# Performance work log

Measured on AMD Instinct MI355X. Metric: run time of the kernel, lower is better.

Reference implementation:

```python
import jax, jax.numpy as jnp
from jax import lax
import numpy as np

BETA = 0.25
K = 64   # num_embeddings
D = 64   # embedding_dim (must equal K per module's view(-1, D))
HID = 128
RES = 64
N_RES = 2


def _conv(x, w, b=None, stride=1, pad=0):
    y = lax.conv_general_dilated(x, w, (stride, stride), [(pad, pad), (pad, pad)],
                                 dimension_numbers=('NCHW', 'OIHW', 'NCHW'))
    if b is not None:
        y = y + b[None, :, None, None]
    return y


def _deconv(x, w, b, stride, pad):
    # torch ConvTranspose2d weight is (Cin, Cout, k, k); emulate via lhs-dilated conv with flipped kernel
    k = w.shape[2]
    p = k - 1 - pad
    w2 = jnp.transpose(w[:, :, ::-1, ::-1], (1, 0, 2, 3))  # -> (Cout, Cin, k, k)
    y = lax.conv_general_dilated(x, w2, (1, 1), [(p, p), (p, p)], lhs_dilation=(stride, stride),
                                 dimension_numbers=('NCHW', 'OIHW', 'NCHW'))
    return y + b[None, :, None, None]


def _res_block(x, w1, w2):
    # [Residual_Layer]*N_RES shares ONE set of weights; in-place ReLU means skip adds relu(x)
    for _ in range(N_RES):
        r = jax.nn.relu(x)
        h = _conv(r, w1, pad=1)
        h = jax.nn.relu(h)
        h = _conv(h, w2)
        x = r + h
    return jax.nn.relu(x)


def setup_inputs() -> dict:
    key = jax.random.key(0)
    ks = jax.random.split(key, 16)
    f32 = jnp.float32
    s = 0.05
    inp = {
        'x': jax.random.normal(ks[0], (32, 1, 256, 256), f32),
        # encoder
        'enc_c1_w': jax.random.normal(ks[1], (HID // 2, 1, 4, 4), f32) * s,
        'enc_c1_b': jnp.zeros((HID // 2,), f32),
        'enc_c2_w': jax.random.normal(ks[2], (HID, HID // 2, 4, 4), f32) * s,
        'enc_c2_b': jnp.zeros((HID,), f32),
        'enc_c3_w': jax.random.normal(ks[3], (HID, HID, 3, 3), f32) * s,
        'enc_c3_b': jnp.zeros((HID,), f32),
        'enc_r1_w': jax.random.normal(ks[4], (RES, HID, 3, 3), f32) * s,
        'enc_r2_w': jax.random.normal(ks[5], (HID, RES, 1, 1), f32) * s,
        # pre-VQ 1x1 conv: hidden -> K channels
        'vqc_w': jax.random.normal(ks[6], (K, HID, 1, 1), f32) * s,
        'vqc_b': jnp.zeros((K,), f32),
        # codebook, uniform(-1/K, 1/K)
        'emb': jax.random.uniform(ks[7], (K, D), f32, -1.0 / K, 1.0 / K),
        # decoder (ConvTranspose2d weights are (Cin, Cout, k, k))
        'dec_c1_w': jax.random.normal(ks[8], (D, HID, 3, 3), f32) * s,
        'dec_c1_b': jnp.zeros((HID,), f32),
        'dec_r1_w': jax.random.normal(ks[9], (RES, HID, 3, 3), f32) * s,
        'dec_r2_w': jax.random.normal(ks[10], (HID, RES, 1, 1), f32) * s,
        'dec_c2_w': jax.random.normal(ks[11], (HID, HID // 2, 4, 4), f32) * s,
        'dec_c2_b': jnp.zeros((HID // 2,), f32),
        'dec_c3_w': jax.random.normal(ks[12], (HID // 2, 1, 4, 4), f32) * s,
        'dec_c3_b': jnp.zeros((1,), f32),
    }
    return inp


def reference(x, enc_c1_w, enc_c1_b, enc_c2_w, enc_c2_b, enc_c3_w, enc_c3_b,
              enc_r1_w, enc_r2_w, vqc_w, vqc_b, emb,
              dec_c1_w, dec_c1_b, dec_r1_w, dec_r2_w, dec_c2_w, dec_c2_b, dec_c3_w, dec_c3_b):
    # ---- encoder ----
    h = jax.nn.relu(_conv(x, enc_c1_w, enc_c1_b, stride=2, pad=1))
    h = jax.nn.relu(_conv(h, enc_c2_w, enc_c2_b, stride=2, pad=1))
    h = _conv(h, enc_c3_w, enc_c3_b, pad=1)
    h = _res_block(h, enc_r1_w, enc_r2_w)
    z = _conv(h, vqc_w, vqc_b)  # (B, K, 64, 64)

    # ---- VQ ----
    zt = jnp.transpose(z, (0, 2, 3, 1))            # (B, H, W, D)
    flat = zt.reshape(-1, D)                        # (N, D)
    dist = (jnp.sum(flat ** 2, axis=1, keepdims=True)
            + jnp.sum(emb ** 2, axis=1)
            - 2.0 * flat @ emb.T)                   # (N, K)
    idx = jnp.argmin(dist, axis=1)                  # (N,)
    onehot = jax.nn.one_hot(idx, K, dtype=flat.dtype)
    q = (onehot @ emb).reshape(zt.shape)
    commitment = jnp.mean((lax.stop_gradient(q) - zt) ** 2)
    embedding_l = jnp.mean((q - lax.stop_gradient(zt)) ** 2)
    loss = commitment * BETA + embedding_l
    q_st = zt + lax.stop_gradient(q - zt)           # straight-through
    mean_enc = jnp.mean(onehot, axis=0)
    perplexity = jnp.exp(-jnp.sum(mean_enc * jnp.log(mean_enc + 1e-10)))
    qn = jnp.transpose(q_st, (0, 3, 1, 2))          # (B, D, 64, 64)

    # ---- decoder ----
    d = _deconv(qn, dec_c1_w, dec_c1_b, 1, 1)
    d = _res_block(d, dec_r1_w, dec_r2_w)
    d = jax.nn.relu(_deconv(d, dec_c2_w, dec_c2_b, 2, 1))
    x_re = jnp.tanh(_deconv(d, dec_c3_w, dec_c3_b, 2, 1))
    return (loss, x_re, perplexity, qn)
```

## Files before the change

### kernel.cpp

```cpp
#include <hip/hip_runtime.h>
#include <cmath>


static constexpr int NPOS  = 131072;
static constexpr long long NELEM = 8388608;

typedef __attribute__((ext_vector_type(8))) short short8;
typedef __attribute__((ext_vector_type(8))) unsigned short ushort8;
typedef __attribute__((ext_vector_type(4))) float f32x4;

__device__ __forceinline__ unsigned short f2bf(float f) {
  unsigned int x = __float_as_uint(f);
  unsigned int r = (x + 0x7fffu + ((x >> 16) & 1u)) >> 16;
  return (unsigned short)r;
}
__device__ __forceinline__ float bf2f(unsigned short u) {
  return __uint_as_float(((unsigned int)u) << 16);
}
__device__ __forceinline__ void split2(float v, unsigned short& h, unsigned short& l) {
  unsigned short hh = f2bf(v);
  h = hh;
  l = f2bf(v - bf2f(hh));
}

__global__ void __launch_bounds__(256) enc1_t(
    const float* __restrict__ in, const float* __restrict__ w,
    const float* __restrict__ bias,
    unsigned short* __restrict__ outh, unsigned short* __restrict__ outl)
{
  int tid = threadIdx.x;
  int rr = tid >> 7, ox = tid & 127;
  int oy  = blockIdx.x * 2 + rr;
  int oc0 = blockIdx.y * 16;
  int b   = blockIdx.z;

  const float* pl = in + (size_t)b * 65536;
  float v[16];
  #pragma unroll
  for (int ky = 0; ky < 4; ++ky) {
    int iy = 2 * oy - 1 + ky;
    #pragma unroll
    for (int kx = 0; kx < 4; ++kx) {
      int ix = 2 * ox - 1 + kx;
      v[ky * 4 + kx] = (iy >= 0 && iy < 256 && ix >= 0 && ix < 256)
                       ? pl[iy * 256 + ix] : 0.f;
    }
  }
  float acc[16];
  #pragma unroll
  for (int o = 0; o < 16; ++o) acc[o] = bias[oc0 + o];
  #pragma unroll
  for (int t = 0; t < 16; ++t)
    #pragma unroll
    for (int o = 0; o < 16; ++o)
      acc[o] += v[t] * w[(size_t)(oc0 + o) * 16 + t];

  size_t o = ((size_t)b * 16900 + (size_t)(oy + 1) * 130 + (ox + 1)) * 64 + oc0;
  ushort8 h0, h1, l0, l1;
  #pragma unroll
  for (int k = 0; k < 8; ++k) {
    unsigned short hh, ll;
    split2(fmaxf(acc[k], 0.f), hh, ll);      h0[k] = hh; l0[k] = ll;
    split2(fmaxf(acc[k + 8], 0.f), hh, ll);  h1[k] = hh; l1[k] = ll;
  }
  *(ushort8*)(outh + o)     = h0;
  *(ushort8*)(outh + o + 8) = h1;
  *(ushort8*)(outl + o)     = l0;
  *(ushort8*)(outl + o + 8) = l1;
}

template<int IC, int OC, int MODE, bool BIAS, bool RELU>
__global__ void __launch_bounds__(256) mfma_enc(
    const unsigned short* __restrict__ inh, const unsigned short* __restrict__ inl,
    const unsigned short* __restrict__ wh, const unsigned short* __restrict__ wl,
    const float* __restrict__ bias,
    const unsigned short* __restrict__ skh, const unsigned short* __restrict__ skl,
    unsigned short* __restrict__ outh, unsigned short* __restrict__ outl)
{
  constexpr int OM = OC / 16;
  constexpr int NT = (MODE == 0) ? 9 : ((MODE == 1) ? 16 : 1);
  constexpr int IW = (MODE == 1) ? 130 : 66;
  const int in_ss  = IW * IW * IC;
  const int out_ss = 4356 * OC;
  const int tid = threadIdx.x;
  const int wv = tid >> 6, lane = tid & 63;
  const int quad = lane >> 4, l15 = lane & 15;
  const int b = blockIdx.z;
  const int y = blockIdx.x * 4 + wv;
  int xs[4];
  #pragma unroll
  for (int j = 0; j < 4; ++j) xs[j] = j * 16 + l15;
  const unsigned short* ibh = inh + (size_t)b * in_ss;
  const unsigned short* ibl = inl + (size_t)b * in_ss;

  f32x4 acc[OM][4];
  #pragma unroll
  for (int m = 0; m < OM; ++m) {
    const int oc0 = m * 16 + quad * 4;
    f32x4 ini = {0.f, 0.f, 0.f, 0.f};
    if (BIAS) {
      float4 bs = *(const float4*)(bias + oc0);
      ini[0] = bs.x; ini[1] = bs.y; ini[2] = bs.z; ini[3] = bs.w;
    }
    #pragma unroll
    for (int j = 0; j < 4; ++j) {
      f32x4 a = ini;
      if (MODE == 2) {
        size_t s = (size_t)b * out_ss + ((size_t)(y + 1) * 66 + (xs[j] + 1)) * OC + oc0;
        ushort4 sh = *(const ushort4*)(skh + s);
        ushort4 sl = *(const ushort4*)(skl + s);
        a[0] += bf2f(sh.x) + bf2f(sl.x);
        a[1] += bf2f(sh.y) + bf2f(sl.y);
        a[2] += bf2f(sh.z) + bf2f(sl.z);
        a[3] += bf2f(sh.w) + bf2f(sl.w);
      }
      acc[m][j] = a;
    }
  }

  for (int t = 0; t < NT; ++t) {
    int off[4];
    #pragma unroll
    for (int j = 0; j < 4; ++j) {
      if (MODE == 1)
        off[j] = ((2 * y + (t >> 2)) * 130 + (2 * xs[j] + (t & 3))) * IC;
      else if (MODE == 0) {
        int dy = t / 3 - 1, dx = t % 3 - 1;
        off[j] = ((y + dy + 1) * 66 + (xs[j] + dx + 1)) * IC;
      } else
        off[j] = ((y + 1) * 66 + (xs[j] + 1)) * IC;
    }
    const unsigned short* wrh = wh + (size_t)t * OC * IC + l15 * IC + quad * 8;
    const unsigned short* wrl = wl + (size_t)t * OC * IC + l15 * IC + quad * 8;
    #pragma unroll
    for (int k0 = 0; k0 < IC; k0 += 32) {
      short8 bh[4], bl[4];
      #pragma unroll
      for (int j = 0; j < 4; ++j) {
        bh[j] = *(const short8*)(ibh + off[j] + quad * 8 + k0);
        bl[j] = *(const short8*)(ibl + off[j] + quad * 8 + k0);
      }
      #pragma unroll
      for (int m = 0; m < OM; ++m) {
        short8 ah = *(const short8*)(wrh + (size_t)m * 16 * IC + k0);
        short8 al = *(const short8*)(wrl + (size_t)m * 16 * IC + k0);
        #pragma unroll
        for (int j = 0; j < 4; ++j) {
          acc[m][j] = __builtin_amdgcn_mfma_f32_16x16x32_bf16(ah, bh[j], acc[m][j], 0, 0, 0);
          acc[m][j] = __builtin_amdgcn_mfma_f32_16x16x32_bf16(ah, bl[j], acc[m][j], 0, 0, 0);
          acc[m][j] = __builtin_amdgcn_mfma_f32_16x16x32_bf16(al, bh[j], acc[m][j], 0, 0, 0);
        }
      }
    }
  }

  #pragma unroll
  for (int m = 0; m < OM; ++m) {
    const int oc0 = m * 16 + quad * 4;
    #pragma unroll
    for (int j = 0; j < 4; ++j) {
      size_t o = (size_t)b * out_ss + ((size_t)(y + 1) * 66 + (xs[j] + 1)) * OC + oc0;
      ushort4 h4, l4;
      unsigned short hh, ll;
      float v;
      v = acc[m][j][0]; if (RELU) v = fmaxf(v, 0.f); split2(v, hh, ll); h4.x = hh; l4.x = ll;
      v = acc[m][j][1]; if (RELU) v = fmaxf(v, 0.f); split2(v, hh, ll); h4.y = hh; l4.y = ll;
      v = acc[m][j][2]; if (RELU) v = fmaxf(v, 0.f); split2(v, hh, ll); h4.z = hh; l4.z = ll;
      v = acc[m][j][3]; if (RELU) v = fmaxf(v, 0.f); split2(v, hh, ll); h4.w = hh; l4.w = ll;
      *(ushort4*)(outh + o) = h4;
      *(ushort4*)(outl + o) = l4;
    }
  }
}

__global__ void __launch_bounds__(256) vq_mfma(
    const unsigned short* __restrict__ xh, const unsigned short* __restrict__ xl,
    const unsigned short* __restrict__ wvh, const unsigned short* __restrict__ wvl,
    const unsigned short* __restrict__ evh, const unsigned short* __restrict__ evl,
    const float* __restrict__ emb, const float* __restrict__ e2,
    const float* __restrict__ vb,
    float* __restrict__ qn, unsigned short* __restrict__ dqb,
    float* __restrict__ sum_sq, int* __restrict__ hist)
{
  __shared__ float zsh[4][16][65];
  __shared__ int lh[64];
  const int tid = threadIdx.x;
  const int wv = tid >> 6, lane = tid & 63;
  const int quad = lane >> 4, l15 = lane & 15;
  const int y = blockIdx.x;
  const int b = blockIdx.z;
  const int x = wv * 16 + l15;
  if (tid < 64) lh[tid] = 0;

  f32x4 zacc[4];
  #pragma unroll
  for (int m = 0; m < 4; ++m) {
    float4 bv = *(const float4*)(vb + m * 16 + quad * 4);
    zacc[m][0] = bv.x; zacc[m][1] = bv.y; zacc[m][2] = bv.z; zacc[m][3] = bv.w;
  }
  size_t xoff = ((size_t)b * 4356 + (size_t)(y + 1) * 66 + (x + 1)) * 128;
  #pragma unroll
  for (int k0 = 0; k0 < 128; k0 += 32) {
    short8 bh = *(const short8*)(xh + xoff + k0 + quad * 8);
    short8 bl = *(const short8*)(xl + xoff + k0 + quad * 8);
    #pragma unroll
    for (int m = 0; m < 4; ++m) {
      short8 ah = *(const short8*)(wvh + (size_t)(m * 16 + l15) * 128 + k0 + quad * 8);
      short8 al = *(const short8*)(wvl + (size_t)(m * 16 + l15) * 128 + k0 + quad * 8);
      zacc[m] = __builtin_amdgcn_mfma_f32_16x16x32_bf16(ah, bh, zacc[m], 0, 0, 0);
      zacc[m] = __builtin_amdgcn_mfma_f32_16x16x32_bf16(ah, bl, zacc[m], 0, 0, 0);
      zacc[m] = __builtin_amdgcn_mfma_f32_16x16x32_bf16(al, bh, zacc[m], 0, 0, 0);
    }
  }

  float z2p = 0.f;
  #pragma unroll
  for (int m = 0; m < 4; ++m)
    #pragma unroll
    for (int r = 0; r < 4; ++r) {
      float zv = zacc[m][r];
      zsh[wv][l15][m * 16 + quad * 4 + r] = zv;
      z2p += zv * zv;
    }
  z2p += __shfl_xor(z2p, 16);
  z2p += __shfl_xor(z2p, 32);
  __syncthreads();

  f32x4 dacc[4];
  #pragma unroll
  for (int m = 0; m < 4; ++m) { dacc[m][0]=0.f; dacc[m][1]=0.f; dacc[m][2]=0.f; dacc[m][3]=0.f; }
  #pragma unroll
  for (int k0 = 0; k0 < 64; k0 += 32) {
    short8 bh, bl;
    #pragma unroll
    for (int j = 0; j < 8; ++j) {
      float zv = zsh[wv][l15][k0 + quad * 8 + j];
      unsigned short hh, ll;
      split2(zv, hh, ll);
      bh[j] = (short)hh; bl[j] = (short)ll;
    }
    #pragma unroll
    for (int m = 0; m < 4; ++m) {
      short8 ah = *(const short8*)(evh + (size_t)(m * 16 + l15) * 64 + k0 + quad * 8);
      short8 al = *(const short8*)(evl + (size_t)(m * 16 + l15) * 64 + k0 + quad * 8);
      dacc[m] = __builtin_amdgcn_mfma_f32_16x16x32_bf16(ah, bh, dacc[m], 0, 0, 0);
      dacc[m] = __builtin_amdgcn_mfma_f32_16x16x32_bf16(ah, bl, dacc[m], 0, 0, 0);
      dacc[m] = __builtin_amdgcn_mfma_f32_16x16x32_bf16(al, bh, dacc[m], 0, 0, 0);
    }
  }

  float best = INFINITY;
  int bidx = 64;
  #pragma unroll
  for (int m = 0; m < 4; ++m) {
    float4 e2v = *(const float4*)(e2 + m * 16 + quad * 4);
    #pragma unroll
    for (int r = 0; r < 4; ++r) {
      float e2s = (r == 0) ? e2v.x : (r == 1) ? e2v.y : (r == 2) ? e2v.z : e2v.w;
      float d = z2p + e2s - 2.f * dacc[m][r];
      int code = m * 16 + quad * 4 + r;
      if (d < best || (d == best && code < bidx)) { best = d; bidx = code; }
    }
  }
  {
    float ob = __shfl_xor(best, 16);
    int   oi = __shfl_xor(bidx, 16);
    if (ob < best || (ob == best && oi < bidx)) { best = ob; bidx = oi; }
    ob = __shfl_xor(best, 32);
    oi = __shfl_xor(bidx, 32);
    if (ob < best || (ob == best && oi < bidx)) { best = ob; bidx = oi; }
  }

  float ev[16];
  #pragma unroll
  for (int i = 0; i < 4; ++i) {
    float4 t = *(const float4*)(emb + (size_t)bidx * 64 + quad * 16 + i * 4);
    ev[i * 4] = t.x; ev[i * 4 + 1] = t.y; ev[i * 4 + 2] = t.z; ev[i * 4 + 3] = t.w;
  }
  float sq = 0.f;
  #pragma unroll
  for (int i = 0; i < 16; ++i) {
    float zv = zsh[wv][l15][quad * 16 + i];
    float df = ev[i] - zv;
    sq += df * df;
  }
  #pragma unroll
  for (int off = 1; off < 64; off <<= 1) sq += __shfl_xor(sq, off);
  if (lane == 0) atomicAdd(sum_sq, sq);
  if (quad == 0) atomicAdd(&lh[bidx], 1);

  int pos = y * 64 + x;
  float* qb = qn + (size_t)b * 262144 + (size_t)(quad * 16) * 4096 + pos;
  #pragma unroll
  for (int i = 0; i < 16; ++i) qb[(size_t)i * 4096] = ev[i];

  unsigned short* dq = dqb + ((size_t)b * 4356 + (size_t)(y + 1) * 66 + (x + 1)) * 64 + quad * 16;
  ushort8 d0, d1;
  #pragma unroll
  for (int i = 0; i < 8; ++i) { d0[i] = f2bf(ev[i]); d1[i] = f2bf(ev[i + 8]); }
  *(ushort8*)dq = d0;
  *(ushort8*)(dq + 8) = d1;

  __syncthreads();
  if (tid < 64) atomicAdd(&hist[tid], lh[tid]);
}

template<int IC, int OC, int MODE, bool HAS_BIAS, bool HAS_SKIP, bool RELU>
__global__ void __launch_bounds__(256) mfma_conv(
    const unsigned short* __restrict__ in, const unsigned short* __restrict__ wt,
    const float* __restrict__ bias, const unsigned short* __restrict__ skip,
    unsigned short* __restrict__ out, int in_ss, int out_ss)
{
  constexpr int OM = OC / 16;
  constexpr int NT = (MODE == 0) ? 9 : ((MODE == 1) ? 4 : 1);
  int ry = 0, rx = 0;
  if (MODE == 1) {
    int p = blockIdx.y;
    ry = p >> 1; rx = p & 1;
    wt  += (size_t)p * 4 * OC * IC;
    out += (size_t)p * 4356 * OC;
  }
  const int tid = threadIdx.x;
  const int wv = tid >> 6, lane = tid & 63;
  const int quad = lane >> 4, l15 = lane & 15;
  const int b = blockIdx.z;
  const int y = blockIdx.x * 4 + wv;
  int xs[4];
  #pragma unroll
  for (int j = 0; j < 4; ++j) xs[j] = j * 16 + l15;
  const unsigned short* inb = in + (size_t)b * (size_t)in_ss;

  f32x4 acc[OM][4];
  #pragma unroll
  for (int m = 0; m < OM; ++m) {
    const int oc0 = m * 16 + quad * 4;
    f32x4 ini = {0.f, 0.f, 0.f, 0.f};
    if (HAS_BIAS) {
      float4 bs = *(const float4*)(bias + oc0);
      ini[0] = bs.x; ini[1] = bs.y; ini[2] = bs.z; ini[3] = bs.w;
    }
    #pragma unroll
    for (int j = 0; j < 4; ++j) {
      f32x4 a = ini;
      if (HAS_SKIP) {
        size_t s = (size_t)b * (size_t)out_ss + ((size_t)(y + 1) * 66 + (xs[j] + 1)) * OC + oc0;
        ushort4 sv = *(const ushort4*)(skip + s);
        a[0] += bf2f(sv.x); a[1] += bf2f(sv.y); a[2] += bf2f(sv.z); a[3] += bf2f(sv.w);
      }
      acc[m][j] = a;
    }
  }

  #pragma unroll
  for (int t = 0; t < NT; ++t) {
    const int dy = (MODE == 0) ? (t / 3 - 1) : ((MODE == 1) ? (ry - (t >> 1)) : 0);
    const int dx = (MODE == 0) ? (t % 3 - 1) : ((MODE == 1) ? (rx - (t & 1)) : 0);
    const unsigned short* wr = wt + (size_t)t * OC * IC + (size_t)l15 * IC + quad * 8;
    #pragma unroll
    for (int k0 = 0; k0 < IC; k0 += 32) {
      short8 fb[4];
      #pragma unroll
      for (int j = 0; j < 4; ++j)
        fb[j] = *(const short8*)(inb + ((size_t)(y + dy + 1) * 66 + (xs[j] + dx + 1)) * IC + quad * 8 + k0);
      #pragma unroll
      for (int m = 0; m < OM; ++m) {
        short8 fa = *(const short8*)(wr + (size_t)m * 16 * IC + k0);
        #pragma unroll
        for (int j = 0; j < 4; ++j)
          acc[m][j] = __builtin_amdgcn_mfma_f32_16x16x32_bf16(fa, fb[j], acc[m][j], 0, 0, 0);
      }
    }
  }

  #pragma unroll
  for (int m = 0; m < OM; ++m) {
    const int oc0 = m * 16 + quad * 4;
    #pragma unroll
    for (int j = 0; j < 4; ++j) {
      unsigned short* o = out + (size_t)b * (size_t)out_ss
                        + ((size_t)(y + 1) * 66 + (xs[j] + 1)) * OC + oc0;
      ushort4 u4;
      float v;
      v = acc[m][j][0]; if (RELU) v = fmaxf(v, 0.f); u4.x = f2bf(v);
      v = acc[m][j][1]; if (RELU) v = fmaxf(v, 0.f); u4.y = f2bf(v);
      v = acc[m][j][2]; if (RELU) v = fmaxf(v, 0.f); u4.z = f2bf(v);
      v = acc[m][j][3]; if (RELU) v = fmaxf(v, 0.f); u4.w = f2bf(v);
      *(ushort4*)o = u4;
    }
  }
}

__global__ void __launch_bounds__(256) dec3_t(
    const unsigned short* __restrict__ p4, const float* __restrict__ w,
    const float* __restrict__ bias, float* __restrict__ out)
{
  int tid = threadIdx.x;
  int yr = tid >> 7, x = tid & 127;
  int y  = blockIdx.x * 2 + yr;
  int b  = blockIdx.z;

  const int kt[2][2] = {{1, 3}, {0, 2}};
  const int dt[2][2] = {{1, 0}, {2, 1}};

  const unsigned short* base[9];
  #pragma unroll
  for (int dy = 0; dy < 3; ++dy) {
    int iy = y + dy - 1;
    int py = iy & 1, u = iy >> 1;
    #pragma unroll
    for (int dx = 0; dx < 3; ++dx) {
      int ix = x + dx - 1;
      int px = ix & 1, v = ix >> 1;
      base[dy * 3 + dx] = p4 + ((size_t)(b * 4 + py * 2 + px) * 4356
                                + (size_t)(u + 1) * 66 + (v + 1)) * 64;
    }
  }

  float acc[4] = {0.f, 0.f, 0.f, 0.f};
  for (int oct = 0; oct < 8; ++oct) {
    ushort8 s[9];
    #pragma unroll
    for (int t = 0; t < 9; ++t)
      s[t] = *(const ushort8*)(base[t] + oct * 8);

    #pragma unroll
    for (int j = 0; j < 8; ++j) {
      const float* wp = w + (size_t)(oct * 8 + j) * 16;
      float v9[9];
      #pragma unroll
      for (int t = 0; t < 9; ++t) v9[t] = bf2f(s[t][j]);
      #pragma unroll
      for (int ry = 0; ry < 2; ++ry)
        #pragma unroll
        for (int rx = 0; rx < 2; ++rx)
          #pragma unroll
          for (int a = 0; a < 2; ++a)
            #pragma unroll
            for (int c2 = 0; c2 < 2; ++c2)
              acc[ry * 2 + rx] += v9[dt[ry][a] * 3 + dt[rx][c2]]
                                * wp[kt[ry][a] * 4 + kt[rx][c2]];
    }
  }

  float b0 = bias[0];
  float* ob = out + (size_t)b * 65536;
  #pragma unroll
  for (int ry = 0; ry < 2; ++ry)
    #pragma unroll
    for (int rx = 0; rx < 2; ++rx)
      ob[(2 * y + ry) * 256 + 2 * x + rx] = tanhf(acc[ry * 2 + rx] + b0);
}

struct RingArgs {
  unsigned short* p[5];
  int icl[5];
  int H[5];
  int planes[5];
};
__global__ void rings_k(RingArgs a)
{
  int bi = blockIdx.y;
  if ((int)blockIdx.x >= a.planes[bi]) return;
  int H = a.H[bi];
  int icl = a.icl[bi];
  int C = 1 << icl;
  unsigned short* pl = a.p[bi] + (size_t)blockIdx.x * H * H * C;
  int cells = 4 * H - 4;
  int total = cells * C;
  for (int idx = threadIdx.x; idx < total; idx += 256) {
    int cell = idx >> icl;
    int e = idx & (C - 1);
    int row, col;
    if (cell < H)             { row = 0;     col = cell; }
    else if (cell < 2 * H)    { row = H - 1; col = cell - H; }
    else if (cell < 2 * H + (H - 2)) { row = cell - 2 * H + 1; col = 0; }
    else                      { row = cell - 2 * H - (H - 2) + 1; col = H - 1; }
    pl[((size_t)row * H + col) * C + e] = 0;
  }
}

__global__ void repack_k(const float* __restrict__ c1w, const float* __restrict__ r1w,
                         const float* __restrict__ r2w, const float* __restrict__ c2w,
                         unsigned short* __restrict__ W)
{
  int idx = blockIdx.x * 256 + threadIdx.x;
  if (idx >= 286720) return;
  float val;
  if (idx < 73728) {
    int t = idx / 8192, rem = idx & 8191;
    int oc = rem >> 6, ic = rem & 63;
    int ky = t / 3, kx = t - ky * 3;
    val = c1w[((ic * 128 + oc) * 3 + (2 - ky)) * 3 + (2 - kx)];
  } else if (idx < 147456) {
    int j = idx - 73728;
    int t = j / 8192, rem = j & 8191;
    int oc = rem >> 7, ic = rem & 127;
    int ky = t / 3, kx = t - ky * 3;
    val = r1w[((oc * 128 + ic) * 3 + ky) * 3 + kx];
  } else if (idx < 155648) {
    int j = idx - 147456;
    int oc = j >> 6, ic = j & 63;
    val = r2w[oc * 64 + ic];
  } else {
    int j = idx - 155648;
    int p = j >> 15;
    int t2 = (j >> 13) & 3;
    int oc = (j >> 7) & 63;
    int ic = j & 127;
    int ry = p >> 1, rx = p & 1;
    int aY = t2 >> 1, aX = t2 & 1;
    int ky = aY ? (3 - ry) : (1 - ry);
    int kx = aX ? (3 - rx) : (1 - rx);
    val = c2w[((ic * 64 + oc) * 4 + ky) * 4 + kx];
  }
  W[idx] = f2bf(val);
}

__global__ void repack_enc_k(const float* __restrict__ c2w, const float* __restrict__ c3w,
                             const float* __restrict__ r1w, const float* __restrict__ r2w,
                             unsigned short* __restrict__ Wh, unsigned short* __restrict__ Wl)
{
  int idx = blockIdx.x * 256 + threadIdx.x;
  if (idx >= 360448) return;
  float val;
  if (idx < 131072) {
    int t = idx >> 13;
    int rem = idx & 8191;
    int oc = rem >> 6, ic = rem & 63;
    val = c2w[(((size_t)oc * 64 + ic) << 4) + t];
  } else if (idx < 278528) {
    int j = idx - 131072;
    int t = j / 16384;
    int rem = j & 16383;
    int oc = rem >> 7, ic = rem & 127;
    val = c3w[((size_t)oc * 128 + ic) * 9 + t];
  } else if (idx < 352256) {
    int j = idx - 278528;
    int t = j / 8192;
    int rem = j & 8191;
    int oc = rem >> 7, ic = rem & 127;
    val = r1w[((size_t)oc * 128 + ic) * 9 + t];
  } else {
    int j = idx - 352256;
    int oc = j >> 6, ic = j & 63;
    val = r2w[oc * 64 + ic];
  }
  unsigned short h = f2bf(val);
  Wh[idx] = h;
  Wl[idx] = f2bf(val - bf2f(h));
}

__global__ void repack_vq_k(const float* __restrict__ vqw, const float* __restrict__ emb,
                            unsigned short* __restrict__ wvh, unsigned short* __restrict__ wvl,
                            unsigned short* __restrict__ evh, unsigned short* __restrict__ evl,
                            float* __restrict__ e2)
{
  int idx = blockIdx.x * 256 + threadIdx.x;
  if (idx < 8192) {
    float v = vqw[idx];
    unsigned short h = f2bf(v);
    wvh[idx] = h;
    wvl[idx] = f2bf(v - bf2f(h));
  } else if (idx < 12288) {
    int j = idx - 8192;
    float v = emb[j];
    unsigned short h = f2bf(v);
    evh[j] = h;
    evl[j] = f2bf(v - bf2f(h));
  }
  if (idx < 64) {
    float s = 0.f;
    for (int d = 0; d < 64; ++d) { float e = emb[idx * 64 + d]; s += e * e; }
    e2[idx] = s;
  }
}

__global__ void init_k(float* sum_sq, int* hist)
{
  int t = threadIdx.x;
  if (t == 0) sum_sq[0] = 0.f;
  if (t < 64) hist[t] = 0;
}

__global__ void finalize_k(const float* __restrict__ sum_sq, const int* __restrict__ hist,
                           float* __restrict__ loss_out, float* __restrict__ perp_out)
{
  if (threadIdx.x == 0) {
    float mse = sum_sq[0] / (float)NELEM;
    loss_out[0] = 1.25f * mse;
    float ent = 0.f;
    for (int k = 0; k < 64; ++k) {
      float p = (float)hist[k] / (float)NPOS;
      ent += p * logf(p + 1e-10f);
    }
    perp_out[0] = expf(-ent);
  }
}

extern "C" void kernel_launch(void* const* d_in, const int* in_sizes, int n_in,
                              void* d_out, int out_size, void* d_ws, size_t ws_size,
                              hipStream_t stream)
{
  const float* x        = (const float*)d_in[0];
  const float* enc_c1_w = (const float*)d_in[1];
  const float* enc_c1_b = (const float*)d_in[2];
  const float* enc_c2_w = (const float*)d_in[3];
  const float* enc_c2_b = (const float*)d_in[4];
  const float* enc_c3_w = (const float*)d_in[5];
  const float* enc_c3_b = (const float*)d_in[6];
  const float* enc_r1_w = (const float*)d_in[7];
  const float* enc_r2_w = (const float*)d_in[8];
  const float* vqc_w    = (const float*)d_in[9];
  const float* vqc_b    = (const float*)d_in[10];
  const float* emb      = (const float*)d_in[11];
  const float* dec_c1_w = (const float*)d_in[12];
  const float* dec_c1_b = (const float*)d_in[13];
  const float* dec_r1_w = (const float*)d_in[14];
  const float* dec_r2_w = (const float*)d_in[15];
  const float* dec_c2_w = (const float*)d_in[16];
  const float* dec_c2_b = (const float*)d_in[17];
  const float* dec_c3_w = (const float*)d_in[18];
  const float* dec_c3_b = (const float*)d_in[19];

  float* out      = (float*)d_out;
  float* loss_out = out;
  float* xre_out  = out + 1;
  float* perp_out = out + 1 + 2097152;
  float* qn_out   = out + 2 + 2097152;

  float* sum_sq = (float*)d_ws;
  int*   hist   = (int*)d_ws + 1;
  char*  pool   = (char*)d_ws + 1024;

  unsigned short* Wd  = (unsigned short*)(pool + 0);
  unsigned short* Weh = (unsigned short*)(pool + 600000);
  unsigned short* Wel = (unsigned short*)(pool + 1400000);
  unsigned short* Wvh = (unsigned short*)(pool + 2121728);
  unsigned short* Wvl = (unsigned short*)(pool + 2138112);
  unsigned short* Evh = (unsigned short*)(pool + 2154496);
  unsigned short* Evl = (unsigned short*)(pool + 2162688);
  float*          E2  = (float*)(pool + 2170880);
  unsigned short* E1h = (unsigned short*)(pool + 2200000);
  unsigned short* E1l = (unsigned short*)(pool + 71500000);
  unsigned short* B2h = (unsigned short*)(pool + 141000000);
  unsigned short* B2l = (unsigned short*)(pool + 177000000);
  unsigned short* R0h = (unsigned short*)(pool + 2200000);
  unsigned short* R0l = (unsigned short*)(pool + 38000000);
  unsigned short* Hh  = (unsigned short*)(pool + 74000000);
  unsigned short* Hl  = (unsigned short*)(pool + 92000000);
  unsigned short* X1h = (unsigned short*)(pool + 141000000);
  unsigned short* X1l = (unsigned short*)(pool + 177000000);
  unsigned short* X2h = (unsigned short*)(pool + 2200000);
  unsigned short* X2l = (unsigned short*)(pool + 38000000);
  unsigned short* Dq  = (unsigned short*)(pool + 213000000);
  unsigned short* Y1  = (unsigned short*)(pool + 141000000);
  unsigned short* S   = (unsigned short*)(pool + 110000000);
  unsigned short* Y2  = (unsigned short*)(pool + 177000000);
  unsigned short* P4  = (unsigned short*)(pool + 2200000);

  const int SS64  = 278784;
  const int SS128 = 557568;
  const int SSP4  = 1115136;

  hipLaunchKernelGGL(init_k, dim3(1), dim3(128), 0, stream, sum_sq, hist);
  hipLaunchKernelGGL(repack_k, dim3(1120), dim3(256), 0, stream,
                     dec_c1_w, dec_r1_w, dec_r2_w, dec_c2_w, Wd);
  hipLaunchKernelGGL(repack_enc_k, dim3(1408), dim3(256), 0, stream,
                     enc_c2_w, enc_c3_w, enc_r1_w, enc_r2_w, Weh, Wel);
  hipLaunchKernelGGL(repack_vq_k, dim3(48), dim3(256), 0, stream,
                     vqc_w, emb, Wvh, Wvl, Evh, Evl, E2);

  {
    RingArgs a;
    a.p[0] = E1h; a.icl[0] = 6; a.H[0] = 130; a.planes[0] = 32;
    a.p[1] = E1l; a.icl[1] = 6; a.H[1] = 130; a.planes[1] = 32;
    a.p[2] = B2h; a.icl[2] = 7; a.H[2] = 66;  a.planes[2] = 32;
    a.p[3] = B2l; a.icl[3] = 7; a.H[3] = 66;  a.planes[3] = 32;
    a.p[4] = Dq;  a.icl[4] = 6; a.H[4] = 66;  a.planes[4] = 32;
    hipLaunchKernelGGL(rings_k, dim3(32, 5), dim3(256), 0, stream, a);
  }

  hipLaunchKernelGGL(enc1_t, dim3(64, 4, 32), dim3(256), 0, stream,
                     x, enc_c1_w, enc_c1_b, E1h, E1l);
  hipLaunchKernelGGL((mfma_enc<64, 128, 1, true, true>),
                     dim3(16, 1, 32), dim3(256), 0, stream,
                     E1h, E1l, Weh, Wel, enc_c2_b, nullptr, nullptr, B2h, B2l);

  {
    RingArgs a;
    a.p[0] = R0h; a.icl[0] = 7; a.H[0] = 66; a.planes[0] = 32;
    a.p[1] = R0l; a.icl[1] = 7; a.H[1] = 66; a.planes[1] = 32;
    a.p[2] = Hh;  a.icl[2] = 6; a.H[2] = 66; a.planes[2] = 32;
    a.p[3] = Hl;  a.icl[3] = 6; a.H[3] = 66; a.planes[3] = 32;
    a.p[4] = S;   a.icl[4] = 6; a.H[4] = 66; a.planes[4] = 32;
    hipLaunchKernelGGL(rings_k, dim3(32, 5), dim3(256), 0, stream, a);
  }

  hipLaunchKernelGGL((mfma_enc<128, 128, 0, true, true>),
                     dim3(16, 1, 32), dim3(256), 0, stream,
                     B2h, B2l, Weh + 131072, Wel + 131072, enc_c3_b,
                     nullptr, nullptr, R0h, R0l);

  {
    RingArgs a;
    a.p[0] = X1h; a.icl[0] = 7; a.H[0] = 66; a.planes[0] = 32;
    a.p[1] = X1l; a.icl[1] = 7; a.H[1] = 66; a.planes[1] = 32;
    a.p[2] = nullptr; a.icl[2] = 0; a.H[2] = 2; a.planes[2] = 0;
    a.p[3] = nullptr; a.icl[3] = 0; a.H[3] = 2; a.planes[3] = 0;
    a.p[4] = nullptr; a.icl[4] = 0; a.H[4] = 2; a.planes[4] = 0;
    hipLaunchKernelGGL(rings_k, dim3(32, 2), dim3(256), 0, stream, a);
  }

  hipLaunchKernelGGL((mfma_enc<128, 64, 0, false, true>),
                     dim3(16, 1, 32), dim3(256), 0, stream,
                     R0h, R0l, Weh + 278528, Wel + 278528, nullptr,
                     nullptr, nullptr, Hh, Hl);
  hipLaunchKernelGGL((mfma_enc<64, 128, 2, false, true>),
                     dim3(16, 1, 32), dim3(256), 0, stream,
                     Hh, Hl, Weh + 352256, Wel + 352256, nullptr,
                     R0h, R0l, X1h, X1l);

  {
    RingArgs a;
    a.p[0] = X2h; a.icl[0] = 7; a.H[0] = 66; a.planes[0] = 32;
    a.p[1] = X2l; a.icl[1] = 7; a.H[1] = 66; a.planes[1] = 32;
    a.p[2] = nullptr; a.icl[2] = 0; a.H[2] = 2; a.planes[2] = 0;
    a.p[3] = nullptr; a.icl[3] = 0; a.H[3] = 2; a.planes[3] = 0;
    a.p[4] = nullptr; a.icl[4] = 0; a.H[4] = 2; a.planes[4] = 0;
    hipLaunchKernelGGL(rings_k, dim3(32, 2), dim3(256), 0, stream, a);
  }

  hipLaunchKernelGGL((mfma_enc<128, 64, 0, false, true>),
                     dim3(16, 1, 32), dim3(256), 0, stream,
                     X1h, X1l, Weh + 278528, Wel + 278528, nullptr,
                     nullptr, nullptr, Hh, Hl);
  hipLaunchKernelGGL((mfma_enc<64, 128, 2, false, true>),
                     dim3(16, 1, 32), dim3(256), 0, stream,
                     Hh, Hl, Weh + 352256, Wel + 352256, nullptr,
                     X1h, X1l, X2h, X2l);

  hipLaunchKernelGGL(vq_mfma, dim3(64, 1, 32), dim3(256), 0, stream,
                     X2h, X2l, Wvh, Wvl, Evh, Evl, emb, E2, vqc_b,
                     qn_out, Dq, sum_sq, hist);

  {
    RingArgs a;
    a.p[0] = Y1;  a.icl[0] = 7; a.H[0] = 66; a.planes[0] = 32;
    a.p[1] = Y2;  a.icl[1] = 7; a.H[1] = 66; a.planes[1] = 32;
    a.p[2] = P4;  a.icl[2] = 6; a.H[2] = 66; a.planes[2] = 128;
    a.p[3] = nullptr; a.icl[3] = 0; a.H[3] = 2; a.planes[3] = 0;
    a.p[4] = nullptr; a.icl[4] = 0; a.H[4] = 2; a.planes[4] = 0;
    hipLaunchKernelGGL(rings_k, dim3(128, 3), dim3(256), 0, stream, a);
  }

  hipLaunchKernelGGL((mfma_conv<64, 128, 0, true, false, true>),
                     dim3(16, 1, 32), dim3(256), 0, stream,
                     Dq, Wd, dec_c1_b, nullptr, Y1, SS64, SS128);
  hipLaunchKernelGGL((mfma_conv<128, 64, 0, false, false, true>),
                     dim3(16, 1, 32), dim3(256), 0, stream,
                     Y1, Wd + 73728, nullptr, nullptr, S, SS128, SS64);
  hipLaunchKernelGGL((mfma_conv<64, 128, 2, false, true, true>),
                     dim3(16, 1, 32), dim3(256), 0, stream,
                     S, Wd + 147456, nullptr, Y1, Y2, SS64, SS128);
  hipLaunchKernelGGL((mfma_conv<128, 64, 0, false, false, true>),
                     dim3(16, 1, 32), dim3(256), 0, stream,
                     Y2, Wd + 73728, nullptr, nullptr, S, SS128, SS64);
  hipLaunchKernelGGL((mfma_conv<64, 128, 2, false, true, true>),
                     dim3(16, 1, 32), dim3(256), 0, stream,
                     S, Wd + 147456, nullptr, Y2, Y1, SS64, SS128);

  hipLaunchKernelGGL((mfma_conv<128, 64, 1, true, false, true>),
                     dim3(16, 4, 32), dim3(256), 0, stream,
                     Y1, Wd + 155648, dec_c2_b, nullptr, P4, SS128, SSP4);

  hipLaunchKernelGGL(dec3_t, dim3(64, 1, 32), dim3(256), 0, stream,
                     P4, dec_c3_w, dec_c3_b, xre_out);

  hipLaunchKernelGGL(finalize_k, dim3(1), dim3(64), 0, stream,
                     sum_sq, hist, loss_out, perp_out);
}
```

Measured before the change: 1.871 ms.

## Split output channels across blocks and remap grid so batches map to XCDs

The MFMA conv kernels now take an OCB template parameter, so layers with 128 output channels run as two blocks of 64 channels each. This doubles the block count and cuts per-thread accumulator registers. The grid is flattened to 1D, with the low 3 bits of the block id selecting the batch within a group of 8, so each XCD handles fixed batch images and their L2-resident data. In exchange, input activations are re-read once per channel block.

```diff
diff --git a/kernel.cpp b/kernel.cpp
--- a/kernel.cpp
+++ b/kernel.cpp
@@ -69,7 +69,7 @@
   *(ushort8*)(outl + o + 8) = l1;
 }
 
-template<int IC, int OC, int MODE, bool BIAS, bool RELU>
+template<int IC, int OC, int OCB, int MODE, bool BIAS, bool RELU>
 __global__ void __launch_bounds__(256) mfma_enc(
     const unsigned short* __restrict__ inh, const unsigned short* __restrict__ inl,
     const unsigned short* __restrict__ wh, const unsigned short* __restrict__ wl,
@@ -77,16 +77,28 @@
     const unsigned short* __restrict__ skh, const unsigned short* __restrict__ skl,
     unsigned short* __restrict__ outh, unsigned short* __restrict__ outl)
 {
-  constexpr int OM = OC / 16;
+  constexpr int OM = OCB / 16;
+  constexpr int NB = OC / OCB;
   constexpr int NT = (MODE == 0) ? 9 : ((MODE == 1) ? 16 : 1);
   constexpr int IW = (MODE == 1) ? 130 : 66;
+  constexpr int PERB = 16 * NB;
   const int in_ss  = IW * IW * IC;
   const int out_ss = 4356 * OC;
   const int tid = threadIdx.x;
   const int wv = tid >> 6, lane = tid & 63;
   const int quad = lane >> 4, l15 = lane & 15;
-  const int b = blockIdx.z;
-  const int y = blockIdx.x * 4 + wv;
+
+  const int id = blockIdx.x;
+  const int xcd = id & 7;
+  const int slot = id >> 3;
+  const int bi = slot / PERB;
+  const int r2 = slot - bi * PERB;
+  const int ocb = r2 >> 4;
+  const int yb  = r2 & 15;
+  const int b = bi * 8 + xcd;
+  const int y = yb * 4 + wv;
+  const int ocbase = ocb * OCB;
+
   int xs[4];
   #pragma unroll
   for (int j = 0; j < 4; ++j) xs[j] = j * 16 + l15;
@@ -96,7 +108,7 @@
   f32x4 acc[OM][4];
   #pragma unroll
   for (int m = 0; m < OM; ++m) {
-    const int oc0 = m * 16 + quad * 4;
+    const int oc0 = ocbase + m * 16 + quad * 4;
     f32x4 ini = {0.f, 0.f, 0.f, 0.f};
     if (BIAS) {
       float4 bs = *(const float4*)(bias + oc0);
@@ -130,8 +142,8 @@
       } else
         off[j] = ((y + 1) * 66 + (xs[j] + 1)) * IC;
     }
-    const unsigned short* wrh = wh + (size_t)t * OC * IC + l15 * IC + quad * 8;
-    const unsigned short* wrl = wl + (size_t)t * OC * IC + l15 * IC + quad * 8;
+    const unsigned short* wrh = wh + (size_t)t * OC * IC + (size_t)(ocbase + l15) * IC + quad * 8;
+    const unsigned short* wrl = wl + (size_t)t * OC * IC + (size_t)(ocbase + l15) * IC + quad * 8;
     #pragma unroll
     for (int k0 = 0; k0 < IC; k0 += 32) {
       short8 bh[4], bl[4];
@@ -156,7 +168,7 @@
 
   #pragma unroll
   for (int m = 0; m < OM; ++m) {
-    const int oc0 = m * 16 + quad * 4;
+    const int oc0 = ocbase + m * 16 + quad * 4;
     #pragma unroll
     for (int j = 0; j < 4; ++j) {
       size_t o = (size_t)b * out_ss + ((size_t)(y + 1) * 66 + (xs[j] + 1)) * OC + oc0;
@@ -305,26 +317,40 @@
   if (tid < 64) atomicAdd(&hist[tid], lh[tid]);
 }
 
-template<int IC, int OC, int MODE, bool HAS_BIAS, bool HAS_SKIP, bool RELU>
+template<int IC, int OC, int OCB, int MODE, bool HAS_BIAS, bool HAS_SKIP, bool RELU>
 __global__ void __launch_bounds__(256) mfma_conv(
     const unsigned short* __restrict__ in, const unsigned short* __restrict__ wt,
     const float* __restrict__ bias, const unsigned short* __restrict__ skip,
     unsigned short* __restrict__ out, int in_ss, int out_ss)
 {
-  constexpr int OM = OC / 16;
+  constexpr int OM = OCB / 16;
+  constexpr int NB = OC / OCB;
   constexpr int NT = (MODE == 0) ? 9 : ((MODE == 1) ? 4 : 1);
+  constexpr int NP = (MODE == 1) ? 4 : 1;
+  constexpr int PERB = 16 * NB * NP;
+  const int tid = threadIdx.x;
+  const int wv = tid >> 6, lane = tid & 63;
+  const int quad = lane >> 4, l15 = lane & 15;
+
+  const int id = blockIdx.x;
+  const int xcd = id & 7;
+  const int slot = id >> 3;
+  const int bi = slot / PERB;
+  int r2 = slot - bi * PERB;
+  int p = 0;
+  if (MODE == 1) { p = r2 / (16 * NB); r2 -= p * (16 * NB); }
+  const int ocb = r2 >> 4;
+  const int yb = r2 & 15;
+  const int b = bi * 8 + xcd;
+  const int y = yb * 4 + wv;
+  const int ocbase = ocb * OCB;
+
   int ry = 0, rx = 0;
   if (MODE == 1) {
-    int p = blockIdx.y;
     ry = p >> 1; rx = p & 1;
     wt  += (size_t)p * 4 * OC * IC;
     out += (size_t)p * 4356 * OC;
   }
-  const int tid = threadIdx.x;
-  const int wv = tid >> 6, lane = tid & 63;
-  const int quad = lane >> 4, l15 = lane & 15;
-  const int b = blockIdx.z;
-  const int y = blockIdx.x * 4 + wv;
   int xs[4];
   #pragma unroll
   for (int j = 0; j < 4; ++j) xs[j] = j * 16 + l15;
@@ -333,7 +359,7 @@
   f32x4 acc[OM][4];
   #pragma unroll
   for (int m = 0; m < OM; ++m) {
-    const int oc0 = m * 16 + quad * 4;
+    const int oc0 = ocbase + m * 16 + quad * 4;
     f32x4 ini = {0.f, 0.f, 0.f, 0.f};
     if (HAS_BIAS) {
       float4 bs = *(const float4*)(bias + oc0);
@@ -355,7 +381,7 @@
   for (int t = 0; t < NT; ++t) {
     const int dy = (MODE == 0) ? (t / 3 - 1) : ((MODE == 1) ? (ry - (t >> 1)) : 0);
     const int dx = (MODE == 0) ? (t % 3 - 1) : ((MODE == 1) ? (rx - (t & 1)) : 0);
-    const unsigned short* wr = wt + (size_t)t * OC * IC + (size_t)l15 * IC + quad * 8;
+    const unsigned short* wr = wt + (size_t)t * OC * IC + (size_t)(ocbase + l15) * IC + quad * 8;
     #pragma unroll
     for (int k0 = 0; k0 < IC; k0 += 32) {
       short8 fb[4];
@@ -374,7 +400,7 @@
 
   #pragma unroll
   for (int m = 0; m < OM; ++m) {
-    const int oc0 = m * 16 + quad * 4;
+    const int oc0 = ocbase + m * 16 + quad * 4;
     #pragma unroll
     for (int j = 0; j < 4; ++j) {
       unsigned short* o = out + (size_t)b * (size_t)out_ss
@@ -682,8 +708,8 @@
 
   hipLaunchKernelGGL(enc1_t, dim3(64, 4, 32), dim3(256), 0, stream,
                      x, enc_c1_w, enc_c1_b, E1h, E1l);
-  hipLaunchKernelGGL((mfma_enc<64, 128, 1, true, true>),
-                     dim3(16, 1, 32), dim3(256), 0, stream,
+  hipLaunchKernelGGL((mfma_enc<64, 128, 64, 1, true, true>),
+                     dim3(1024), dim3(256), 0, stream,
                      E1h, E1l, Weh, Wel, enc_c2_b, nullptr, nullptr, B2h, B2l);
 
   {
@@ -696,8 +722,8 @@
     hipLaunchKernelGGL(rings_k, dim3(32, 5), dim3(256), 0, stream, a);
   }
 
-  hipLaunchKernelGGL((mfma_enc<128, 128, 0, true, true>),
-                     dim3(16, 1, 32), dim3(256), 0, stream,
+  hipLaunchKernelGGL((mfma_enc<128, 128, 64, 0, true, true>),
+                     dim3(1024), dim3(256), 0, stream,
                      B2h, B2l, Weh + 131072, Wel + 131072, enc_c3_b,
                      nullptr, nullptr, R0h, R0l);
 
@@ -711,12 +737,12 @@
     hipLaunchKernelGGL(rings_k, dim3(32, 2), dim3(256), 0, stream, a);
   }
 
-  hipLaunchKernelGGL((mfma_enc<128, 64, 0, false, true>),
-                     dim3(16, 1, 32), dim3(256), 0, stream,
+  hipLaunchKernelGGL((mfma_enc<128, 64, 64, 0, false, true>),
+                     dim3(512), dim3(256), 0, stream,
                      R0h, R0l, Weh + 278528, Wel + 278528, nullptr,
                      nullptr, nullptr, Hh, Hl);
-  hipLaunchKernelGGL((mfma_enc<64, 128, 2, false, true>),
-                     dim3(16, 1, 32), dim3(256), 0, stream,
+  hipLaunchKernelGGL((mfma_enc<64, 128, 64, 2, false, true>),
+                     dim3(1024), dim3(256), 0, stream,
                      Hh, Hl, Weh + 352256, Wel + 352256, nullptr,
                      R0h, R0l, X1h, X1l);
 
@@ -730,12 +756,12 @@
     hipLaunchKernelGGL(rings_k, dim3(32, 2), dim3(256), 0, stream, a);
   }
 
-  hipLaunchKernelGGL((mfma_enc<128, 64, 0, false, true>),
-                     dim3(16, 1, 32), dim3(256), 0, stream,
+  hipLaunchKernelGGL((mfma_enc<128, 64, 64, 0, false, true>),
+                     dim3(512), dim3(256), 0, stream,
                      X1h, X1l, Weh + 278528, Wel + 278528, nullptr,
                      nullptr, nullptr, Hh, Hl);
-  hipLaunchKernelGGL((mfma_enc<64, 128, 2, false, true>),
-                     dim3(16, 1, 32), dim3(256), 0, stream,
+  hipLaunchKernelGGL((mfma_enc<64, 128, 64, 2, false, true>),
+                     dim3(1024), dim3(256), 0, stream,
                      Hh, Hl, Weh + 352256, Wel + 352256, nullptr,
                      X1h, X1l, X2h, X2l);
 
@@ -753,24 +779,24 @@
     hipLaunchKernelGGL(rings_k, dim3(128, 3), dim3(256), 0, stream, a);
   }
 
-  hipLaunchKernelGGL((mfma_conv<64, 128, 0, true, false, true>),
-                     dim3(16, 1, 32), dim3(256), 0, stream,
+  hipLaunchKernelGGL((mfma_conv<64, 128, 64, 0, true, false, true>),
+                     dim3(1024), dim3(256), 0, stream,
                      Dq, Wd, dec_c1_b, nullptr, Y1, SS64, SS128);
-  hipLaunchKernelGGL((mfma_conv<128, 64, 0, false, false, true>),
-                     dim3(16, 1, 32), dim3(256), 0, stream,
+  hipLaunchKernelGGL((mfma_conv<128, 64, 64, 0, false, false, true>),
+                     dim3(512), dim3(256), 0, stream,
                      Y1, Wd + 73728, nullptr, nullptr, S, SS128, SS64);
-  hipLaunchKernelGGL((mfma_conv<64, 128, 2, false, true, true>),
-                     dim3(16, 1, 32), dim3(256), 0, stream,
+  hipLaunchKernelGGL((mfma_conv<64, 128, 64, 2, false, true, true>),
+                     dim3(1024), dim3(256), 0, stream,
                      S, Wd + 147456, nullptr, Y1, Y2, SS64, SS128);
-  hipLaunchKernelGGL((mfma_conv<128, 64, 0, false, false, true>),
-                     dim3(16, 1, 32), dim3(256), 0, stream,
+  hipLaunchKernelGGL((mfma_conv<128, 64, 64, 0, false, false, true>),
+                     dim3(512), dim3(256), 0, stream,
                      Y2, Wd + 73728, nullptr, nullptr, S, SS128, SS64);
-  hipLaunchKernelGGL((mfma_conv<64, 128, 2, false, true, true>),
-                     dim3(16, 1, 32), dim3(256), 0, stream,
+  hipLaunchKernelGGL((mfma_conv<64, 128, 64, 2, false, true, true>),
+                     dim3(1024), dim3(256), 0, stream,
                      S, Wd + 147456, nullptr, Y2, Y1, SS64, SS128);
 
-  hipLaunchKernelGGL((mfma_conv<128, 64, 1, true, false, true>),
-                     dim3(16, 4, 32), dim3(256), 0, stream,
+  hipLaunchKernelGGL((mfma_conv<128, 64, 64, 1, true, false, true>),
+                     dim3(2048), dim3(256), 0, stream,
                      Y1, Wd + 155648, dec_c2_b, nullptr, P4, SS128, SSP4);
 
   hipLaunchKernelGGL(dec3_t, dim3(64, 1, 32), dim3(256), 0, stream,
```

After: 1.923 ms. +2.8%, slower.
